# Kernel optimization log

Hardware: AMD Instinct MI355X
Metric: run time of the kernel (lower is better)

## Reference

```python
import jax, jax.numpy as jnp
import numpy as np

IN_FEATURES = 1024
OUT_FEATURES = 1024
KNOT_COUNT = 5
ORDER = 3
BATCH = 4096


def setup_inputs() -> dict:
    key = jax.random.key(0)
    k1, k2 = jax.random.split(key)
    x = jax.random.normal(k1, (BATCH, IN_FEATURES), dtype=jnp.float32)
    knots = jnp.linspace(-1.0, 1.0, KNOT_COUNT, dtype=jnp.float32)
    coeffs = jax.random.normal(k2, (KNOT_COUNT + ORDER, OUT_FEATURES, IN_FEATURES), dtype=jnp.float32)
    return {"x": x, "knots": knots, "coeffs": coeffs}


def _bspline_bases(x, knots, order):
    # x: [B, I]; knots: [K] uniform grid. Extend to K + 2*order + 1 knots so
    # the number of degree-`order` basis functions is K + order.
    h = knots[1] - knots[0]
    left = knots[0] + h * jnp.arange(-order, 0, dtype=knots.dtype)
    right = knots[-1] + h * jnp.arange(1, order + 2, dtype=knots.dtype)
    t = jnp.concatenate([left, knots, right])  # [K + 2*order + 1]
    xe = x[..., None]  # [B, I, 1]
    # degree-0 indicator bases: [B, I, m-1]
    bases = ((xe >= t[:-1]) & (xe < t[1:])).astype(x.dtype)
    # Cox-de Boor recursion up to degree `order` (vectorized over batch/features)
    for k in range(1, order + 1):
        left_num = (xe - t[: -(k + 1)]) / (t[k:-1] - t[: -(k + 1)])
        right_num = (t[k + 1:] - xe) / (t[k + 1:] - t[1:-k])
        bases = left_num * bases[..., :-1] + right_num * bases[..., 1:]
    return bases  # [B, I, K + order]


def reference(x, knots, coeffs):
    # Faithful fused version of the per-(i,j) python loops:
    # spline_j(b) = sum_n B_n(x[b,i]) * coeffs[n, j, i]; output sums over i.
    bases = _bspline_bases(x, knots, ORDER)          # [B, I, N]
    return jnp.einsum('bin,noi->bo', bases, coeffs)  # [B, O]
```

## Files before the change

### kernel.cpp

```cpp
#include <hip/hip_runtime.h>
#include <hip/hip_bf16.h>
#include <cstdint>
#include <cstddef>

#define IN_F   1024
#define OUT_F  1024
#define NB     8
#define BATCH  4096
#define KTOT   (NB * IN_F)

typedef __attribute__((ext_vector_type(4))) float  f32x4;
typedef __attribute__((ext_vector_type(8))) float  f32x8;
typedef __attribute__((ext_vector_type(8))) __bf16 bf16x8;
typedef __attribute__((ext_vector_type(4))) unsigned short u16x4;

#define GLDS16(g, l)                                                     \
    __builtin_amdgcn_global_load_lds(                                    \
        (const __attribute__((address_space(1))) void*)(g),              \
        (__attribute__((address_space(3))) void*)(l), 16, 0, 0)

__device__ __forceinline__ void spline_w(float r, float w[4]) {
    const float r2 = r * r, r3 = r2 * r;
    const float omr = 1.0f - r;
    w[0] = omr * omr * omr * (1.0f / 6.0f);
    w[1] = (3.0f * r3 - 6.0f * r2 + 4.0f) * (1.0f / 6.0f);
    w[2] = (-3.0f * r3 + 3.0f * r2 + 3.0f * r + 1.0f) * (1.0f / 6.0f);
    w[3] = r3 * (1.0f / 6.0f);
}

__global__ void k_cvt(const float* __restrict__ src, __bf16* __restrict__ dst) {
    const size_t g   = blockIdx.x * blockDim.x + threadIdx.x;
    const size_t idx = g * 8;
    const int i = (int)(idx & 1023);
    const int o = (int)((idx >> 10) & 1023);
    const int c = (i >> 3) & 7;
    const int isw = (i & ~63) | ((c ^ (o & 7)) << 3);
    f32x8 v = *(const f32x8*)(src + idx);
    bf16x8 ov = __builtin_convertvector(v, bf16x8);
    *(bf16x8*)(dst + (idx - i) + isw) = ov;
}

__global__ void k_basis(const float* __restrict__ x, __bf16* __restrict__ A) {
    const int g    = blockIdx.x * blockDim.x + threadIdx.x;
    const int flat = g * 4;
    const int b = flat >> 10, i = flat & 1023;
    f32x4 xv = *(const f32x4*)(x + flat);

    float w[4][4];
    int   jj[4];
#pragma unroll
    for (int e = 0; e < 4; ++e) {
        const float u  = (xv[e] + 2.5f) * 2.0f;
        const float jf = floorf(u);
        jj[e] = (int)jf;
        spline_w(u - jf, w[e]);
    }

    const int c   = (i >> 3) & 7;
    const int isw = (i & ~63) | ((c ^ (b & 7)) << 3) | (i & 7);
    __bf16* base = A + (size_t)b * KTOT + isw;
#pragma unroll
    for (int n = 0; n < NB; ++n) {
        u16x4 pack;
#pragma unroll
        for (int e = 0; e < 4; ++e) {
            const int d = n - jj[e] + 3;
            float v = (d == 0) ? w[e][0]
                    : (d == 1) ? w[e][1]
                    : (d == 2) ? w[e][2]
                    : (d == 3) ? w[e][3] : 0.0f;
            __bf16 h = (__bf16)v;
            pack[e] = __builtin_bit_cast(unsigned short, h);
        }
        *(u16x4*)(base + n * IN_F) = pack;
    }
}

#define BM 128
#define BN 128
#define BK 64
#define NT (KTOT / BK)

__global__ __launch_bounds__(512) void k_gemm(const __bf16* __restrict__ A,
                                              const __bf16* __restrict__ W,
                                              float* __restrict__ C) {
    __shared__ __align__(16) char ls[2][32768];

    const int tid  = threadIdx.x;
    const int o0   = blockIdx.x * BN;
    const int b0   = blockIdx.y * BM;
    const int lane = tid & 63;
    const int wv   = tid >> 6;
    const int wr   = wv >> 2;
    const int wc   = wv & 3;
    const int l15  = lane & 15;
    const int lhi  = lane >> 4;

    f32x4 acc[4][2] = {};

    const int srow  = tid >> 3;
    const int scol8 = (tid & 7) * 8;

    auto STAGE = [&](int buf, int kt) {
        const int k0 = kt * BK;
        const int n  = k0 >> 10;
        const int i0 = k0 & 1023;
        char* la = ls[buf];
        char* lb = ls[buf] + 16384;
#pragma unroll
        for (int it = 0; it < 2; ++it) {
            const __bf16* ga = A + (size_t)(b0 + srow + it * 64) * KTOT + k0 + scol8;
            GLDS16(ga, la + tid * 16 + it * 8192);
        }
#pragma unroll
        for (int it = 0; it < 2; ++it) {
            const __bf16* gw = W + ((size_t)n << 20)
                                 + (size_t)(o0 + srow + it * 64) * IN_F + i0 + scol8;
            GLDS16(gw, lb + tid * 16 + it * 8192);
        }
    };

    STAGE(0, 0);
    __syncthreads();

    int cur = 0;
    for (int kt = 0; kt < NT; ++kt) {
        if (kt + 1 < NT) STAGE(cur ^ 1, kt + 1);
        const char* la = ls[cur];
        const char* lb = ls[cur] + 16384;
#pragma unroll
        for (int kk = 0; kk < BK; kk += 32) {
            bf16x8 af[4], bfr[2];
#pragma unroll
            for (int m = 0; m < 4; ++m) {
                const int r = wr * 64 + m * 16 + l15;
                const int c = ((kk >> 3) + lhi) ^ (r & 7);
                af[m] = *(const bf16x8*)(la + r * 128 + c * 16);
            }
#pragma unroll
            for (int nn = 0; nn < 2; ++nn) {
                const int r = wc * 32 + nn * 16 + l15;
                const int c = ((kk >> 3) + lhi) ^ (r & 7);
                bfr[nn] = *(const bf16x8*)(lb + r * 128 + c * 16);
            }
#pragma unroll
            for (int m = 0; m < 4; ++m)
#pragma unroll
                for (int nn = 0; nn < 2; ++nn)
                    acc[m][nn] = __builtin_amdgcn_mfma_f32_16x16x32_bf16(
                        af[m], bfr[nn], acc[m][nn], 0, 0, 0);
        }
        __syncthreads();
        cur ^= 1;
    }

    const int crow = lhi * 4;
#pragma unroll
    for (int m = 0; m < 4; ++m) {
#pragma unroll
        for (int nn = 0; nn < 2; ++nn) {
            float* cp = C + (size_t)(b0 + wr * 64 + m * 16 + crow) * OUT_F
                          + o0 + wc * 32 + nn * 16 + l15;
#pragma unroll
            for (int j = 0; j < 4; ++j)
                cp[(size_t)j * OUT_F] = acc[m][nn][j];
        }
    }
}

__global__ void k_naive(const float* __restrict__ x, const float* __restrict__ coeffs,
                        float* __restrict__ out) {
    const int b = blockIdx.y * 16 + (threadIdx.x >> 4);
    const int o = blockIdx.x * 16 + (threadIdx.x & 15);
    float sum = 0.0f;
    for (int i = 0; i < IN_F; ++i) {
        const float u  = (x[(size_t)b * IN_F + i] + 2.5f) * 2.0f;
        const float jf = floorf(u);
        const int   j  = (int)jf;
        float w[4];
        spline_w(u - jf, w);
#pragma unroll
        for (int m = 0; m < 4; ++m) {
            const int idx = j - 3 + m;
            if (idx >= 0 && idx < NB)
                sum += w[m] * coeffs[(size_t)idx * OUT_F * IN_F + (size_t)o * IN_F + i];
        }
    }
    out[(size_t)b * OUT_F + o] = sum;
}

extern "C" void kernel_launch(void* const* d_in, const int* in_sizes, int n_in,
                              void* d_out, int out_size, void* d_ws, size_t ws_size,
                              hipStream_t stream) {
    const float* x      = (const float*)d_in[0];
    const float* coeffs = (const float*)d_in[2];
    float* out = (float*)d_out;

    const size_t needA = (size_t)BATCH * KTOT * sizeof(__bf16);
    const size_t needW = (size_t)NB * OUT_F * IN_F * sizeof(__bf16);

    if (ws_size >= needA + needW) {
        __bf16* A  = (__bf16*)d_ws;
        __bf16* Wb = (__bf16*)((char*)d_ws + needA);

        const int cvt_threads = NB * OUT_F * IN_F / 8;
        hipLaunchKernelGGL(k_cvt, dim3(cvt_threads / 256), dim3(256), 0, stream,
                           coeffs, Wb);
        const int bas_threads = BATCH * IN_F / 4;
        hipLaunchKernelGGL(k_basis, dim3(bas_threads / 256), dim3(256), 0, stream,
                           x, A);
        hipLaunchKernelGGL(k_gemm, dim3(OUT_F / BN, BATCH / BM), dim3(512), 0, stream,
                           A, Wb, out);
    } else {
        hipLaunchKernelGGL(k_naive, dim3(OUT_F / 16, BATCH / 16), dim3(256), 0, stream,
                           x, coeffs, out);
    }
}
```

Baseline: 142.0 us.

## Split GEMM reduction dimension in two and sum partials with an add kernel

The bf16 GEMM now runs with a grid z-dimension of 2. Each block handles half of the K tiles, and the second half writes its partial result to a workspace buffer. A new elementwise kernel then adds that partial buffer into the output. The goal is to double the block count so the 256-block grid fills the GPU better and hides latency. The cost is an extra 16 MB partial write, a 32 MB read plus 16 MB write in the add pass, and one more kernel launch. A new fallback branch also runs the conversion and basis kernels needlessly before the naive kernel.

Measured after the change: 132.8 us. -6.5%, faster.

```diff
diff --git a/kernel.cpp b/kernel.cpp
--- a/kernel.cpp
+++ b/kernel.cpp
@@ -80,15 +80,19 @@
 #define BN 128
 #define BK 64
 #define NT (KTOT / BK)
+#define SPLITK 2
+#define NTS (NT / SPLITK)
 
 __global__ __launch_bounds__(512) void k_gemm(const __bf16* __restrict__ A,
                                               const __bf16* __restrict__ W,
-                                              float* __restrict__ C) {
+                                              float* __restrict__ C,
+                                              float* __restrict__ P) {
     __shared__ __align__(16) char ls[2][32768];
 
     const int tid  = threadIdx.x;
     const int o0   = blockIdx.x * BN;
     const int b0   = blockIdx.y * BM;
+    const int kz   = blockIdx.z;
     const int lane = tid & 63;
     const int wv   = tid >> 6;
     const int wr   = wv >> 2;
@@ -120,12 +124,13 @@
         }
     };
 
-    STAGE(0, 0);
+    const int ktBeg = kz * NTS;
+    STAGE(0, ktBeg);
     __syncthreads();
 
     int cur = 0;
-    for (int kt = 0; kt < NT; ++kt) {
-        if (kt + 1 < NT) STAGE(cur ^ 1, kt + 1);
+    for (int kt = ktBeg; kt < ktBeg + NTS; ++kt) {
+        if (kt + 1 < ktBeg + NTS) STAGE(cur ^ 1, kt + 1);
         const char* la = ls[cur];
         const char* lb = ls[cur] + 16384;
 #pragma unroll
@@ -154,18 +159,27 @@
         cur ^= 1;
     }
 
+    float* dst = (kz == 0) ? C : P;
     const int crow = lhi * 4;
 #pragma unroll
     for (int m = 0; m < 4; ++m) {
 #pragma unroll
         for (int nn = 0; nn < 2; ++nn) {
-            float* cp = C + (size_t)(b0 + wr * 64 + m * 16 + crow) * OUT_F
-                          + o0 + wc * 32 + nn * 16 + l15;
+            float* cp = dst + (size_t)(b0 + wr * 64 + m * 16 + crow) * OUT_F
+                            + o0 + wc * 32 + nn * 16 + l15;
 #pragma unroll
             for (int j = 0; j < 4; ++j)
                 cp[(size_t)j * OUT_F] = acc[m][nn][j];
         }
     }
+}
+
+__global__ void k_add(float* __restrict__ C, const float* __restrict__ P) {
+    const size_t g = (size_t)(blockIdx.x * blockDim.x + threadIdx.x) * 4;
+    f32x4 a = *(const f32x4*)(C + g);
+    f32x4 b = *(const f32x4*)(P + g);
+    a += b;
+    *(f32x4*)(C + g) = a;
 }
 
 __global__ void k_naive(const float* __restrict__ x, const float* __restrict__ coeffs,
@@ -198,21 +212,32 @@
 
     const size_t needA = (size_t)BATCH * KTOT * sizeof(__bf16);
     const size_t needW = (size_t)NB * OUT_F * IN_F * sizeof(__bf16);
-
-    if (ws_size >= needA + needW) {
+    const size_t needP = (size_t)BATCH * OUT_F * sizeof(float);
+
+    if (ws_size >= needA + needW + needP) {
         __bf16* A  = (__bf16*)d_ws;
         __bf16* Wb = (__bf16*)((char*)d_ws + needA);
-
-        const int cvt_threads = NB * OUT_F * IN_F / 8;
-        hipLaunchKernelGGL(k_cvt, dim3(cvt_threads / 256), dim3(256), 0, stream,
-                           coeffs, Wb);
-        const int bas_threads = BATCH * IN_F / 4;
-        hipLaunchKernelGGL(k_basis, dim3(bas_threads / 256), dim3(256), 0, stream,
-                           x, A);
-        hipLaunchKernelGGL(k_gemm, dim3(OUT_F / BN, BATCH / BM), dim3(512), 0, stream,
-                           A, Wb, out);
+        float*  P  = (float*)((char*)d_ws + needA + needW);
+
+        hipLaunchKernelGGL(k_cvt, dim3(NB * OUT_F * IN_F / 8 / 256), dim3(256), 0,
+                           stream, coeffs, Wb);
+        hipLaunchKernelGGL(k_basis, dim3(BATCH * IN_F / 4 / 256), dim3(256), 0,
+                           stream, x, A);
+        hipLaunchKernelGGL(k_gemm, dim3(OUT_F / BN, BATCH / BM, SPLITK), dim3(512),
+                           0, stream, A, Wb, out, P);
+        hipLaunchKernelGGL(k_add, dim3(BATCH * OUT_F / 4 / 256), dim3(256), 0,
+                           stream, out, P);
+    } else if (ws_size >= needA + needW) {
+        __bf16* A  = (__bf16*)d_ws;
+        __bf16* Wb = (__bf16*)((char*)d_ws + needA);
+        hipLaunchKernelGGL(k_cvt, dim3(NB * OUT_F * IN_F / 8 / 256), dim3(256), 0,
+                           stream, coeffs, Wb);
+        hipLaunchKernelGGL(k_basis, dim3(BATCH * IN_F / 4 / 256), dim3(256), 0,
+                           stream, x, A);
+        hipLaunchKernelGGL(k_naive, dim3(OUT_F / 16, BATCH / 16), dim3(256), 0,
+                           stream, x, coeffs, out);
     } else {
-        hipLaunchKernelGGL(k_naive, dim3(OUT_F / 16, BATCH / 16), dim3(256), 0, stream,
-                           x, coeffs, out);
-    }
-}
+        hipLaunchKernelGGL(k_naive, dim3(OUT_F / 16, BATCH / 16), dim3(256), 0,
+                           stream, x, coeffs, out);
+    }
+}
```

## Deepen GEMM LDS pipeline to four buffers with manual vmcnt waits

Applied to the files above, without the earlier changes.

The GEMM moves from a double-buffered LDS scheme to a four-buffer ring with a prefetch distance of three K-tiles. It uses explicit s_waitcnt vmcnt counts and a single raw s_barrier per iteration in place of the two __syncthreads. The aim is to hide more global-to-LDS latency and cut barrier overhead per tile. The cost is 128KB of LDS per block, which likely limits each CU to one resident block instead of two and so lowers occupancy. The launch code is only reformatted.

New measurement: 124.0 us. 12.7% less time.

```diff
diff --git a/kernel.cpp b/kernel.cpp
--- a/kernel.cpp
+++ b/kernel.cpp
@@ -80,11 +80,12 @@
 #define BN 128
 #define BK 64
 #define NT (KTOT / BK)
+#define NBUF 4
 
 __global__ __launch_bounds__(512) void k_gemm(const __bf16* __restrict__ A,
                                               const __bf16* __restrict__ W,
                                               float* __restrict__ C) {
-    __shared__ __align__(16) char ls[2][32768];
+    __shared__ __align__(16) char ls[NBUF][32768];
 
     const int tid  = threadIdx.x;
     const int o0   = blockIdx.x * BN;
@@ -121,13 +122,20 @@
     };
 
     STAGE(0, 0);
-    __syncthreads();
-
-    int cur = 0;
-    for (int kt = 0; kt < NT; ++kt) {
-        if (kt + 1 < NT) STAGE(cur ^ 1, kt + 1);
-        const char* la = ls[cur];
-        const char* lb = ls[cur] + 16384;
+    STAGE(1, 1);
+    STAGE(2, 2);
+
+    for (int t = 0; t < NT; ++t) {
+        if (t < NT - 2)       asm volatile("s_waitcnt vmcnt(8)" ::: "memory");
+        else if (t == NT - 2) asm volatile("s_waitcnt vmcnt(4)" ::: "memory");
+        else                  asm volatile("s_waitcnt vmcnt(0)" ::: "memory");
+        __builtin_amdgcn_s_barrier();
+        __builtin_amdgcn_sched_barrier(0);
+
+        if (t + 3 < NT) STAGE((t + 3) & (NBUF - 1), t + 3);
+
+        const char* la = ls[t & (NBUF - 1)];
+        const char* lb = la + 16384;
 #pragma unroll
         for (int kk = 0; kk < BK; kk += 32) {
             bf16x8 af[4], bfr[2];
@@ -150,8 +158,6 @@
                     acc[m][nn] = __builtin_amdgcn_mfma_f32_16x16x32_bf16(
                         af[m], bfr[nn], acc[m][nn], 0, 0, 0);
         }
-        __syncthreads();
-        cur ^= 1;
     }
 
     const int crow = lhi * 4;
@@ -203,16 +209,14 @@
         __bf16* A  = (__bf16*)d_ws;
         __bf16* Wb = (__bf16*)((char*)d_ws + needA);
 
-        const int cvt_threads = NB * OUT_F * IN_F / 8;
-        hipLaunchKernelGGL(k_cvt, dim3(cvt_threads / 256), dim3(256), 0, stream,
-                           coeffs, Wb);
-        const int bas_threads = BATCH * IN_F / 4;
-        hipLaunchKernelGGL(k_basis, dim3(bas_threads / 256), dim3(256), 0, stream,
-                           x, A);
-        hipLaunchKernelGGL(k_gemm, dim3(OUT_F / BN, BATCH / BM), dim3(512), 0, stream,
-                           A, Wb, out);
+        hipLaunchKernelGGL(k_cvt, dim3(NB * OUT_F * IN_F / 8 / 256), dim3(256), 0,
+                           stream, coeffs, Wb);
+        hipLaunchKernelGGL(k_basis, dim3(BATCH * IN_F / 4 / 256), dim3(256), 0,
+                           stream, x, A);
+        hipLaunchKernelGGL(k_gemm, dim3(OUT_F / BN, BATCH / BM), dim3(512),
+                           0, stream, A, Wb, out);
     } else {
-        hipLaunchKernelGGL(k_naive, dim3(OUT_F / 16, BATCH / 16), dim3(256), 0, stream,
-                           x, coeffs, out);
-    }
-}
+        hipLaunchKernelGGL(k_naive, dim3(OUT_F / 16, BATCH / 16), dim3(256), 0,
+                           stream, x, coeffs, out);
+    }
+}
```
